# Kernel tuning notes

Hardware: AMD Instinct MI355X
Metric: run time of the kernel (lower is better)

Reference implementation:

```python
import jax, jax.numpy as jnp
import numpy as np

N_NODES = 50000
N_EDGES = 800000
IN_CH = 128
HID = 128
N_GRAPHS = 512


def setup_inputs() -> dict:
    key = jax.random.key(0)
    ks = jax.random.split(key, 12)
    x = jax.random.normal(ks[0], (N_NODES, IN_CH), dtype=jnp.float32)
    edge_index = jax.random.randint(ks[1], (2, N_EDGES), 0, N_NODES, dtype=jnp.int64)
    batch = jnp.sort(jax.random.randint(ks[2], (N_NODES,), 0, N_GRAPHS, dtype=jnp.int64))
    s = 0.05
    params = {
        'W1l': jax.random.normal(ks[3], (HID, IN_CH), dtype=jnp.float32) * s,
        'W1r': jax.random.normal(ks[4], (HID, IN_CH), dtype=jnp.float32) * s,
        'b1': jax.random.normal(ks[5], (HID,), dtype=jnp.float32) * s,
        'W2l': jax.random.normal(ks[6], (HID, HID), dtype=jnp.float32) * s,
        'W2r': jax.random.normal(ks[7], (HID, HID), dtype=jnp.float32) * s,
        'b2': jax.random.normal(ks[8], (HID,), dtype=jnp.float32) * s,
        'W3l': jax.random.normal(ks[9], (HID, HID), dtype=jnp.float32) * s,
        'W3r': jax.random.normal(ks[10], (HID, HID), dtype=jnp.float32) * s,
        'b3': jax.random.normal(ks[11], (HID,), dtype=jnp.float32) * s,
    }
    return {'x': x, 'edge_index': edge_index, 'batch': batch, **params}


def reference(x, edge_index, batch, W1l, W1r, b1, W2l, W2r, b2, W3l, W3r, b3):
    src = edge_index[0]
    dst = edge_index[1]
    n = x.shape[0]
    # in-degree for mean aggregation (nodes with no in-edges get 0 aggregate)
    deg = jax.ops.segment_sum(jnp.ones((src.shape[0],), x.dtype), dst, num_segments=n)
    inv_deg = (1.0 / jnp.maximum(deg, 1.0))[:, None]  # [N,1]

    def sage(h, Wl, Wr, b):
        # gather neighbor feats, scatter-mean to targets, then linear + root term
        agg = jax.ops.segment_sum(h[src], dst, num_segments=n) * inv_deg  # [N,d]
        return agg @ Wl.T + h @ Wr.T + b

    h = jax.nn.relu(sage(x, W1l, W1r, b1))
    h = jax.nn.relu(sage(h, W2l, W2r, b2))
    h = jax.nn.relu(sage(h, W3l, W3r, b3))

    # global mean pool over graph ids
    counts = jax.ops.segment_sum(jnp.ones((n,), h.dtype), batch, num_segments=N_GRAPHS)
    pooled = jax.ops.segment_sum(h, batch, num_segments=N_GRAPHS)
    return pooled / jnp.maximum(counts, 1.0)[:, None]
```

## Files before the change

kernel.cpp:

```cpp
#include <hip/hip_runtime.h>

#define N_NODES 50000
#define NP 50048
#define N_EDGES 800000
#define N_GRAPHS 512
#define F 128
#define SCAN_BLOCKS 196

typedef __bf16 bf16x8 __attribute__((ext_vector_type(8)));
typedef float f32x4 __attribute__((ext_vector_type(4)));
typedef unsigned short ushort_t;
typedef unsigned int uint_t;

__device__ inline ushort_t f2bf(float f) {
    uint_t u = __float_as_uint(f);
    u += 0x7FFFu + ((u >> 16) & 1u);
    return (ushort_t)(u >> 16);
}
__device__ inline float bf2f(ushort_t u) {
    return __uint_as_float(((uint_t)u) << 16);
}

__global__ __launch_bounds__(256) void k_castx(const float* __restrict__ x,
                                               ushort_t* __restrict__ X) {
    int i = (blockIdx.x * 256 + threadIdx.x) * 4;
    if (i >= NP * F) return;
    uint_t lo = 0, hi = 0;
    if (i < N_NODES * F) {
        float4 v = *(const float4*)&x[i];
        lo = (uint_t)f2bf(v.x) | ((uint_t)f2bf(v.y) << 16);
        hi = (uint_t)f2bf(v.z) | ((uint_t)f2bf(v.w) << 16);
    }
    *(uint2*)&X[i] = make_uint2(lo, hi);
}

__global__ __launch_bounds__(256) void k_castw(const float* __restrict__ w0,
                                               const float* __restrict__ w1,
                                               const float* __restrict__ w2,
                                               const float* __restrict__ w3,
                                               const float* __restrict__ w4,
                                               const float* __restrict__ w5,
                                               ushort_t* __restrict__ W) {
    int idx = blockIdx.x * 256 + threadIdx.x;
    if (idx >= 6 * 4096) return;
    int m = idx >> 12;
    int o = (idx & 4095) * 4;
    const float* src = w0;
    if (m == 1) src = w1; else if (m == 2) src = w2; else if (m == 3) src = w3;
    else if (m == 4) src = w4; else if (m == 5) src = w5;
    float4 v = *(const float4*)&src[o];
    uint_t lo = (uint_t)f2bf(v.x) | ((uint_t)f2bf(v.y) << 16);
    uint_t hi = (uint_t)f2bf(v.z) | ((uint_t)f2bf(v.w) << 16);
    *(uint2*)&W[m * 16384 + o] = make_uint2(lo, hi);
}

__global__ __launch_bounds__(256) void k_deg(const int* __restrict__ dst,
                                             int* __restrict__ deg) {
    int e = blockIdx.x * 256 + threadIdx.x;
    if (e < N_EDGES) atomicAdd(&deg[dst[e]], 1);
}

__global__ __launch_bounds__(256) void k_scan1(const int* __restrict__ deg,
                                               int* __restrict__ part) {
    __shared__ int s[256];
    int i = blockIdx.x * 256 + threadIdx.x;
    s[threadIdx.x] = (i < N_NODES) ? deg[i] : 0;
    __syncthreads();
#pragma unroll
    for (int st = 128; st > 0; st >>= 1) {
        if (threadIdx.x < st) s[threadIdx.x] += s[threadIdx.x + st];
        __syncthreads();
    }
    if (threadIdx.x == 0) part[blockIdx.x] = s[0];
}

__global__ void k_scan2(int* __restrict__ part, int* __restrict__ offs) {
    if (threadIdx.x == 0) {
        int acc = 0;
        for (int i = 0; i < SCAN_BLOCKS; i++) {
            int v = part[i];
            part[i] = acc;
            acc += v;
        }
        offs[N_NODES] = N_EDGES;
    }
}

__global__ __launch_bounds__(256) void k_scan3(const int* __restrict__ deg,
                                               const int* __restrict__ part,
                                               int* __restrict__ offs,
                                               int* __restrict__ cursor) {
    __shared__ int s[256];
    int tid = threadIdx.x;
    int i = blockIdx.x * 256 + tid;
    int v = (i < N_NODES) ? deg[i] : 0;
    s[tid] = v;
    __syncthreads();
#pragma unroll
    for (int st = 1; st < 256; st <<= 1) {
        int add = (tid >= st) ? s[tid - st] : 0;
        __syncthreads();
        s[tid] += add;
        __syncthreads();
    }
    if (i < N_NODES) {
        int off = s[tid] - v + part[blockIdx.x];
        offs[i] = off;
        cursor[i] = off;
    }
}

__global__ __launch_bounds__(256) void k_fill(const int* __restrict__ src,
                                              const int* __restrict__ dst,
                                              int* __restrict__ cursor,
                                              int* __restrict__ csr) {
    int e = blockIdx.x * 256 + threadIdx.x;
    if (e < N_EDGES) {
        int pos = atomicAdd(&cursor[dst[e]], 1);
        csr[pos] = src[e];
    }
}

__global__ __launch_bounds__(256) void k_gather(const ushort_t* __restrict__ h,
                                                const int* __restrict__ csr,
                                                const int* __restrict__ offs,
                                                ushort_t* __restrict__ agg) {
    int t = blockIdx.x * 256 + threadIdx.x;
    int n = t >> 4;
    int lane = t & 15;
    if (n >= N_NODES) return;
    int lo = offs[n], hi = offs[n + 1];
    const uint4* h4 = (const uint4*)h;
    float ax[8], ay[8];
#pragma unroll
    for (int j = 0; j < 8; j++) { ax[j] = 0.f; ay[j] = 0.f; }
    int i = lo;
    for (; i + 2 <= hi; i += 2) {
        int s0 = csr[i], s1 = csr[i + 1];
        uint4 v0 = h4[(size_t)s0 * 16 + lane];
        uint4 v1 = h4[(size_t)s1 * 16 + lane];
        ax[0] += __uint_as_float(v0.x << 16); ax[1] += __uint_as_float(v0.x & 0xFFFF0000u);
        ax[2] += __uint_as_float(v0.y << 16); ax[3] += __uint_as_float(v0.y & 0xFFFF0000u);
        ax[4] += __uint_as_float(v0.z << 16); ax[5] += __uint_as_float(v0.z & 0xFFFF0000u);
        ax[6] += __uint_as_float(v0.w << 16); ax[7] += __uint_as_float(v0.w & 0xFFFF0000u);
        ay[0] += __uint_as_float(v1.x << 16); ay[1] += __uint_as_float(v1.x & 0xFFFF0000u);
        ay[2] += __uint_as_float(v1.y << 16); ay[3] += __uint_as_float(v1.y & 0xFFFF0000u);
        ay[4] += __uint_as_float(v1.z << 16); ay[5] += __uint_as_float(v1.z & 0xFFFF0000u);
        ay[6] += __uint_as_float(v1.w << 16); ay[7] += __uint_as_float(v1.w & 0xFFFF0000u);
    }
    if (i < hi) {
        int s0 = csr[i];
        uint4 v0 = h4[(size_t)s0 * 16 + lane];
        ax[0] += __uint_as_float(v0.x << 16); ax[1] += __uint_as_float(v0.x & 0xFFFF0000u);
        ax[2] += __uint_as_float(v0.y << 16); ax[3] += __uint_as_float(v0.y & 0xFFFF0000u);
        ax[4] += __uint_as_float(v0.z << 16); ax[5] += __uint_as_float(v0.z & 0xFFFF0000u);
        ax[6] += __uint_as_float(v0.w << 16); ax[7] += __uint_as_float(v0.w & 0xFFFF0000u);
    }
    float sc = 1.0f / fmaxf((float)(hi - lo), 1.0f);
    uint_t r[4];
#pragma unroll
    for (int j = 0; j < 4; j++) {
        ushort_t e0 = f2bf((ax[2 * j] + ay[2 * j]) * sc);
        ushort_t e1 = f2bf((ax[2 * j + 1] + ay[2 * j + 1]) * sc);
        r[j] = (uint_t)e0 | ((uint_t)e1 << 16);
    }
    ((uint4*)agg)[(size_t)n * 16 + lane] = make_uint4(r[0], r[1], r[2], r[3]);
}

__global__ __launch_bounds__(256) void k_linear(const ushort_t* __restrict__ agg,
                                                const ushort_t* h,
                                                const ushort_t* __restrict__ Wl,
                                                const ushort_t* __restrict__ Wr,
                                                const float* __restrict__ bias,
                                                ushort_t* out) {
    __shared__ uint4 Alds4[512];
    __shared__ uint4 Blds4[512];
    ushort_t* Alds = (ushort_t*)Alds4;
    ushort_t* Blds = (ushort_t*)Blds4;

    int t = threadIdx.x;
    int w = t >> 6;
    int lane = t & 63;
    int bm = blockIdx.x * 128;
    int wm = (w & 1) * 64;
    int wn = (w >> 1) * 64;
    int lrow = lane & 15;
    int kg = lane >> 4;

    f32x4 acc[4][4];
#pragma unroll
    for (int i = 0; i < 4; i++)
#pragma unroll
        for (int j = 0; j < 4; j++) acc[i][j] = (f32x4){0.f, 0.f, 0.f, 0.f};

    for (int kk = 0; kk < 256; kk += 32) {
        const ushort_t* A = (kk < 128) ? agg : h;
        const ushort_t* W = (kk < 128) ? Wl : Wr;
        int k0 = kk & 127;

        __syncthreads();
#pragma unroll
        for (int p = 0; p < 2; p++) {
            int s = p * 256 + t;
            int chunk = s >> 7;
            int row = s & 127;
            const ushort_t* gA = A + (size_t)(bm + row) * F + k0 + chunk * 8;
            const ushort_t* gB = W + (size_t)row * F + k0 + chunk * 8;
            ushort_t* lA = Alds + (size_t)((p * 4 + w) * 64) * 8;
            ushort_t* lB = Blds + (size_t)((p * 4 + w) * 64) * 8;
            __builtin_amdgcn_global_load_lds(
                (const __attribute__((address_space(1))) void*)gA,
                (__attribute__((address_space(3))) void*)lA, 16, 0, 0);
            __builtin_amdgcn_global_load_lds(
                (const __attribute__((address_space(1))) void*)gB,
                (__attribute__((address_space(3))) void*)lB, 16, 0, 0);
        }
        __syncthreads();

        bf16x8 af[4], bfr[4];
#pragma unroll
        for (int i = 0; i < 4; i++)
            af[i] = *(const bf16x8*)(Alds + (size_t)(kg * 128 + wm + i * 16 + lrow) * 8);
#pragma unroll
        for (int j = 0; j < 4; j++)
            bfr[j] = *(const bf16x8*)(Blds + (size_t)(kg * 128 + wn + j * 16 + lrow) * 8);
#pragma unroll
        for (int i = 0; i < 4; i++)
#pragma unroll
            for (int j = 0; j < 4; j++)
                acc[i][j] = __builtin_amdgcn_mfma_f32_16x16x32_bf16(
                    af[i], bfr[j], acc[i][j], 0, 0, 0);
    }

    int quad = lane >> 4;
#pragma unroll
    for (int j = 0; j < 4; j++) {
        int c = wn + j * 16 + lrow;
        float bj = bias[c];
#pragma unroll
        for (int i = 0; i < 4; i++) {
#pragma unroll
            for (int r = 0; r < 4; r++) {
                int row = bm + wm + i * 16 + quad * 4 + r;
                if (row < N_NODES) {
                    float v = fmaxf(acc[i][j][r] + bj, 0.0f);
                    out[(size_t)row * F + c] = f2bf(v);
                }
            }
        }
    }
}

__global__ __launch_bounds__(128) void k_pool(const ushort_t* __restrict__ h,
                                              const int* __restrict__ batch,
                                              float* __restrict__ out) {
    int g = blockIdx.x;
    int j = threadIdx.x;
    int lo = 0, hi = N_NODES;
    while (lo < hi) {
        int m = (lo + hi) >> 1;
        if (batch[m] < g) lo = m + 1; else hi = m;
    }
    int start = lo;
    lo = start; hi = N_NODES;
    while (lo < hi) {
        int m = (lo + hi) >> 1;
        if (batch[m] < g + 1) lo = m + 1; else hi = m;
    }
    int end = lo;
    float s = 0.0f;
    for (int n = start; n < end; n++) s += bf2f(h[(size_t)n * F + j]);
    out[g * F + j] = s / fmaxf((float)(end - start), 1.0f);
}

extern "C" void kernel_launch(void* const* d_in, const int* in_sizes, int n_in,
                              void* d_out, int out_size, void* d_ws, size_t ws_size,
                              hipStream_t stream) {
    const float* x   = (const float*)d_in[0];
    const int*   ei  = (const int*)d_in[1];
    const int* batch = (const int*)d_in[2];
    const float* W1l = (const float*)d_in[3];
    const float* W1r = (const float*)d_in[4];
    const float* b1  = (const float*)d_in[5];
    const float* W2l = (const float*)d_in[6];
    const float* W2r = (const float*)d_in[7];
    const float* b2  = (const float*)d_in[8];
    const float* W3l = (const float*)d_in[9];
    const float* W3r = (const float*)d_in[10];
    const float* b3  = (const float*)d_in[11];
    float* out = (float*)d_out;

    const int* src = ei;
    const int* dst = ei + N_EDGES;

    ushort_t* X   = (ushort_t*)d_ws;
    ushort_t* H   = X + (size_t)NP * F;
    ushort_t* AGG = H + (size_t)NP * F;
    ushort_t* WB  = AGG + (size_t)NP * F;
    int* iw = (int*)(WB + 6 * 16384);
    int* ideg   = iw;
    int* offs   = ideg + N_NODES;
    int* cursor = offs + N_NODES + 1;
    int* part   = cursor + N_NODES;
    int* csr    = part + 256;

    const ushort_t* Wb1l = WB;
    const ushort_t* Wb1r = WB + 16384;
    const ushort_t* Wb2l = WB + 2 * 16384;
    const ushort_t* Wb2r = WB + 3 * 16384;
    const ushort_t* Wb3l = WB + 4 * 16384;
    const ushort_t* Wb3r = WB + 5 * 16384;

    k_castx<<<(NP * F / 4 + 255) / 256, 256, 0, stream>>>(x, X);
    k_castw<<<(6 * 4096 + 255) / 256, 256, 0, stream>>>(W1l, W1r, W2l, W2r, W3l, W3r, WB);

    hipMemsetAsync(ideg, 0, N_NODES * sizeof(int), stream);
    k_deg<<<(N_EDGES + 255) / 256, 256, 0, stream>>>(dst, ideg);
    k_scan1<<<SCAN_BLOCKS, 256, 0, stream>>>(ideg, part);
    k_scan2<<<1, 64, 0, stream>>>(part, offs);
    k_scan3<<<SCAN_BLOCKS, 256, 0, stream>>>(ideg, part, offs, cursor);
    k_fill<<<(N_EDGES + 255) / 256, 256, 0, stream>>>(src, dst, cursor, csr);

    const int gatherBlocks = (N_NODES * 16 + 255) / 256;
    const int linearBlocks = NP / 128;

    k_gather<<<gatherBlocks, 256, 0, stream>>>(X, csr, offs, AGG);
    k_linear<<<linearBlocks, 256, 0, stream>>>(AGG, X, Wb1l, Wb1r, b1, H);
    k_gather<<<gatherBlocks, 256, 0, stream>>>(H, csr, offs, AGG);
    k_linear<<<linearBlocks, 256, 0, stream>>>(AGG, H, Wb2l, Wb2r, b2, H);
    k_gather<<<gatherBlocks, 256, 0, stream>>>(H, csr, offs, AGG);
    k_linear<<<linearBlocks, 256, 0, stream>>>(AGG, H, Wb3l, Wb3r, b3, H);

    k_pool<<<N_GRAPHS, 128, 0, stream>>>(H, batch, out);
}
```

Before: 378.4 us.

## Fuse prep kernels, unroll gather by four, retile linear to 64-row blocks

Merges the x cast, weight cast and degree-count kernels into one launch to cut launch overhead. The gather loop now issues four neighbour row loads per iteration instead of two, giving more memory-level parallelism. The linear kernel moves to 64-row tiles with a K-step of 64, doubling the block count and halving the per-wave accumulator count. The cost is a larger B tile in LDS and more B-tile reloads per output row.

```diff
diff --git a/kernel.cpp b/kernel.cpp
--- a/kernel.cpp
+++ b/kernel.cpp
@@ -6,6 +6,9 @@
 #define N_GRAPHS 512
 #define F 128
 #define SCAN_BLOCKS 196
+#define CASTX_BLOCKS 6256
+#define CASTW_BLOCKS 96
+#define DEG_BLOCKS 3125
 
 typedef __bf16 bf16x8 __attribute__((ext_vector_type(8)));
 typedef float f32x4 __attribute__((ext_vector_type(4)));
@@ -21,43 +24,40 @@
     return __uint_as_float(((uint_t)u) << 16);
 }
 
-__global__ __launch_bounds__(256) void k_castx(const float* __restrict__ x,
-                                               ushort_t* __restrict__ X) {
-    int i = (blockIdx.x * 256 + threadIdx.x) * 4;
-    if (i >= NP * F) return;
-    uint_t lo = 0, hi = 0;
-    if (i < N_NODES * F) {
-        float4 v = *(const float4*)&x[i];
-        lo = (uint_t)f2bf(v.x) | ((uint_t)f2bf(v.y) << 16);
-        hi = (uint_t)f2bf(v.z) | ((uint_t)f2bf(v.w) << 16);
-    }
-    *(uint2*)&X[i] = make_uint2(lo, hi);
-}
-
-__global__ __launch_bounds__(256) void k_castw(const float* __restrict__ w0,
-                                               const float* __restrict__ w1,
-                                               const float* __restrict__ w2,
-                                               const float* __restrict__ w3,
-                                               const float* __restrict__ w4,
-                                               const float* __restrict__ w5,
-                                               ushort_t* __restrict__ W) {
-    int idx = blockIdx.x * 256 + threadIdx.x;
-    if (idx >= 6 * 4096) return;
-    int m = idx >> 12;
-    int o = (idx & 4095) * 4;
-    const float* src = w0;
-    if (m == 1) src = w1; else if (m == 2) src = w2; else if (m == 3) src = w3;
-    else if (m == 4) src = w4; else if (m == 5) src = w5;
-    float4 v = *(const float4*)&src[o];
-    uint_t lo = (uint_t)f2bf(v.x) | ((uint_t)f2bf(v.y) << 16);
-    uint_t hi = (uint_t)f2bf(v.z) | ((uint_t)f2bf(v.w) << 16);
-    *(uint2*)&W[m * 16384 + o] = make_uint2(lo, hi);
-}
-
-__global__ __launch_bounds__(256) void k_deg(const int* __restrict__ dst,
-                                             int* __restrict__ deg) {
-    int e = blockIdx.x * 256 + threadIdx.x;
-    if (e < N_EDGES) atomicAdd(&deg[dst[e]], 1);
+__global__ __launch_bounds__(256) void k_prep(
+    const float* __restrict__ x,
+    const float* __restrict__ w0, const float* __restrict__ w1,
+    const float* __restrict__ w2, const float* __restrict__ w3,
+    const float* __restrict__ w4, const float* __restrict__ w5,
+    const int* __restrict__ dst,
+    ushort_t* __restrict__ X, ushort_t* __restrict__ WB,
+    int* __restrict__ ideg) {
+    int b = blockIdx.x;
+    int t = threadIdx.x;
+    if (b < CASTX_BLOCKS) {
+        int i = (b * 256 + t) * 4;
+        uint_t lo = 0, hi = 0;
+        if (i < N_NODES * F) {
+            float4 v = *(const float4*)&x[i];
+            lo = (uint_t)f2bf(v.x) | ((uint_t)f2bf(v.y) << 16);
+            hi = (uint_t)f2bf(v.z) | ((uint_t)f2bf(v.w) << 16);
+        }
+        *(uint2*)&X[i] = make_uint2(lo, hi);
+    } else if (b < CASTX_BLOCKS + CASTW_BLOCKS) {
+        int idx = (b - CASTX_BLOCKS) * 256 + t;
+        int m = idx >> 12;
+        int o = (idx & 4095) * 4;
+        const float* src = w0;
+        if (m == 1) src = w1; else if (m == 2) src = w2; else if (m == 3) src = w3;
+        else if (m == 4) src = w4; else if (m == 5) src = w5;
+        float4 v = *(const float4*)&src[o];
+        uint_t lo = (uint_t)f2bf(v.x) | ((uint_t)f2bf(v.y) << 16);
+        uint_t hi = (uint_t)f2bf(v.z) | ((uint_t)f2bf(v.w) << 16);
+        *(uint2*)&WB[m * 16384 + o] = make_uint2(lo, hi);
+    } else {
+        int e = (b - CASTX_BLOCKS - CASTW_BLOCKS) * 256 + t;
+        atomicAdd(&ideg[dst[e]], 1);
+    }
 }
 
 __global__ __launch_bounds__(256) void k_scan1(const int* __restrict__ deg,
@@ -119,6 +119,13 @@
         int pos = atomicAdd(&cursor[dst[e]], 1);
         csr[pos] = src[e];
     }
+}
+
+__device__ inline void addrow(float* a, uint4 v) {
+    a[0] += __uint_as_float(v.x << 16); a[1] += __uint_as_float(v.x & 0xFFFF0000u);
+    a[2] += __uint_as_float(v.y << 16); a[3] += __uint_as_float(v.y & 0xFFFF0000u);
+    a[4] += __uint_as_float(v.z << 16); a[5] += __uint_as_float(v.z & 0xFFFF0000u);
+    a[6] += __uint_as_float(v.w << 16); a[7] += __uint_as_float(v.w & 0xFFFF0000u);
 }
 
 __global__ __launch_bounds__(256) void k_gather(const ushort_t* __restrict__ h,
@@ -135,26 +142,18 @@
 #pragma unroll
     for (int j = 0; j < 8; j++) { ax[j] = 0.f; ay[j] = 0.f; }
     int i = lo;
-    for (; i + 2 <= hi; i += 2) {
-        int s0 = csr[i], s1 = csr[i + 1];
+    for (; i + 4 <= hi; i += 4) {
+        int s0 = csr[i], s1 = csr[i + 1], s2 = csr[i + 2], s3 = csr[i + 3];
         uint4 v0 = h4[(size_t)s0 * 16 + lane];
         uint4 v1 = h4[(size_t)s1 * 16 + lane];
-        ax[0] += __uint_as_float(v0.x << 16); ax[1] += __uint_as_float(v0.x & 0xFFFF0000u);
-        ax[2] += __uint_as_float(v0.y << 16); ax[3] += __uint_as_float(v0.y & 0xFFFF0000u);
-        ax[4] += __uint_as_float(v0.z << 16); ax[5] += __uint_as_float(v0.z & 0xFFFF0000u);
-        ax[6] += __uint_as_float(v0.w << 16); ax[7] += __uint_as_float(v0.w & 0xFFFF0000u);
-        ay[0] += __uint_as_float(v1.x << 16); ay[1] += __uint_as_float(v1.x & 0xFFFF0000u);
-        ay[2] += __uint_as_float(v1.y << 16); ay[3] += __uint_as_float(v1.y & 0xFFFF0000u);
-        ay[4] += __uint_as_float(v1.z << 16); ay[5] += __uint_as_float(v1.z & 0xFFFF0000u);
-        ay[6] += __uint_as_float(v1.w << 16); ay[7] += __uint_as_float(v1.w & 0xFFFF0000u);
-    }
-    if (i < hi) {
+        uint4 v2 = h4[(size_t)s2 * 16 + lane];
+        uint4 v3 = h4[(size_t)s3 * 16 + lane];
+        addrow(ax, v0); addrow(ay, v1); addrow(ax, v2); addrow(ay, v3);
+    }
+    for (; i < hi; i++) {
         int s0 = csr[i];
         uint4 v0 = h4[(size_t)s0 * 16 + lane];
-        ax[0] += __uint_as_float(v0.x << 16); ax[1] += __uint_as_float(v0.x & 0xFFFF0000u);
-        ax[2] += __uint_as_float(v0.y << 16); ax[3] += __uint_as_float(v0.y & 0xFFFF0000u);
-        ax[4] += __uint_as_float(v0.z << 16); ax[5] += __uint_as_float(v0.z & 0xFFFF0000u);
-        ax[6] += __uint_as_float(v0.w << 16); ax[7] += __uint_as_float(v0.w & 0xFFFF0000u);
+        addrow(ax, v0);
     }
     float sc = 1.0f / fmaxf((float)(hi - lo), 1.0f);
     uint_t r[4];
@@ -174,26 +173,27 @@
                                                 const float* __restrict__ bias,
                                                 ushort_t* out) {
     __shared__ uint4 Alds4[512];
-    __shared__ uint4 Blds4[512];
+    __shared__ uint4 Blds4[1024];
     ushort_t* Alds = (ushort_t*)Alds4;
     ushort_t* Blds = (ushort_t*)Blds4;
 
     int t = threadIdx.x;
     int w = t >> 6;
     int lane = t & 63;
-    int bm = blockIdx.x * 128;
-    int wm = (w & 1) * 64;
+    int bm = blockIdx.x * 64;
+    int wm = (w & 1) * 32;
     int wn = (w >> 1) * 64;
     int lrow = lane & 15;
     int kg = lane >> 4;
 
-    f32x4 acc[4][4];
-#pragma unroll
-    for (int i = 0; i < 4; i++)
+    f32x4 acc[2][4];
+#pragma unroll
+    for (int i = 0; i < 2; i++)
 #pragma unroll
         for (int j = 0; j < 4; j++) acc[i][j] = (f32x4){0.f, 0.f, 0.f, 0.f};
 
-    for (int kk = 0; kk < 256; kk += 32) {
+    for (int iter = 0; iter < 4; iter++) {
+        int kk = iter * 64;
         const ushort_t* A = (kk < 128) ? agg : h;
         const ushort_t* W = (kk < 128) ? Wl : Wr;
         int k0 = kk & 127;
@@ -201,35 +201,43 @@
         __syncthreads();
 #pragma unroll
         for (int p = 0; p < 2; p++) {
-            int s = p * 256 + t;
-            int chunk = s >> 7;
-            int row = s & 127;
-            const ushort_t* gA = A + (size_t)(bm + row) * F + k0 + chunk * 8;
-            const ushort_t* gB = W + (size_t)row * F + k0 + chunk * 8;
-            ushort_t* lA = Alds + (size_t)((p * 4 + w) * 64) * 8;
-            ushort_t* lB = Blds + (size_t)((p * 4 + w) * 64) * 8;
+            int chunkA = p * 4 + w;
+            const ushort_t* gA = A + (size_t)(bm + lane) * F + k0 + chunkA * 8;
+            ushort_t* lA = Alds + (size_t)(chunkA * 64) * 8;
             __builtin_amdgcn_global_load_lds(
                 (const __attribute__((address_space(1))) void*)gA,
                 (__attribute__((address_space(3))) void*)lA, 16, 0, 0);
+        }
+#pragma unroll
+        for (int p = 0; p < 4; p++) {
+            int chunkB = p * 2 + (w >> 1);
+            int rbase = (w & 1) * 64;
+            const ushort_t* gB = W + (size_t)(rbase + lane) * F + k0 + chunkB * 8;
+            ushort_t* lB = Blds + (size_t)(chunkB * 128 + rbase) * 8;
             __builtin_amdgcn_global_load_lds(
                 (const __attribute__((address_space(1))) void*)gB,
                 (__attribute__((address_space(3))) void*)lB, 16, 0, 0);
         }
         __syncthreads();
 
-        bf16x8 af[4], bfr[4];
-#pragma unroll
-        for (int i = 0; i < 4; i++)
-            af[i] = *(const bf16x8*)(Alds + (size_t)(kg * 128 + wm + i * 16 + lrow) * 8);
-#pragma unroll
-        for (int j = 0; j < 4; j++)
-            bfr[j] = *(const bf16x8*)(Blds + (size_t)(kg * 128 + wn + j * 16 + lrow) * 8);
-#pragma unroll
-        for (int i = 0; i < 4; i++)
+#pragma unroll
+        for (int ks = 0; ks < 2; ks++) {
+            bf16x8 af[2], bfr[4];
+#pragma unroll
+            for (int i = 0; i < 2; i++)
+                af[i] = *(const bf16x8*)(Alds +
+                    (size_t)((ks * 4 + kg) * 64 + wm + i * 16 + lrow) * 8);
 #pragma unroll
             for (int j = 0; j < 4; j++)
-                acc[i][j] = __builtin_amdgcn_mfma_f32_16x16x32_bf16(
-                    af[i], bfr[j], acc[i][j], 0, 0, 0);
+                bfr[j] = *(const bf16x8*)(Blds +
+                    (size_t)((ks * 4 + kg) * 128 + wn + j * 16 + lrow) * 8);
+#pragma unroll
+            for (int i = 0; i < 2; i++)
+#pragma unroll
+                for (int j = 0; j < 4; j++)
+                    acc[i][j] = __builtin_amdgcn_mfma_f32_16x16x32_bf16(
+                        af[i], bfr[j], acc[i][j], 0, 0, 0);
+        }
     }
 
     int quad = lane >> 4;
@@ -238,7 +246,7 @@
         int c = wn + j * 16 + lrow;
         float bj = bias[c];
 #pragma unroll
-        for (int i = 0; i < 4; i++) {
+        for (int i = 0; i < 2; i++) {
 #pragma unroll
             for (int r = 0; r < 4; r++) {
                 int row = bm + wm + i * 16 + quad * 4 + r;
@@ -311,18 +319,16 @@
     const ushort_t* Wb3l = WB + 4 * 16384;
     const ushort_t* Wb3r = WB + 5 * 16384;
 
-    k_castx<<<(NP * F / 4 + 255) / 256, 256, 0, stream>>>(x, X);
-    k_castw<<<(6 * 4096 + 255) / 256, 256, 0, stream>>>(W1l, W1r, W2l, W2r, W3l, W3r, WB);
-
     hipMemsetAsync(ideg, 0, N_NODES * sizeof(int), stream);
-    k_deg<<<(N_EDGES + 255) / 256, 256, 0, stream>>>(dst, ideg);
+    k_prep<<<CASTX_BLOCKS + CASTW_BLOCKS + DEG_BLOCKS, 256, 0, stream>>>(
+        x, W1l, W1r, W2l, W2r, W3l, W3r, dst, X, WB, ideg);
     k_scan1<<<SCAN_BLOCKS, 256, 0, stream>>>(ideg, part);
     k_scan2<<<1, 64, 0, stream>>>(part, offs);
     k_scan3<<<SCAN_BLOCKS, 256, 0, stream>>>(ideg, part, offs, cursor);
     k_fill<<<(N_EDGES + 255) / 256, 256, 0, stream>>>(src, dst, cursor, csr);
 
     const int gatherBlocks = (N_NODES * 16 + 255) / 256;
-    const int linearBlocks = NP / 128;
+    const int linearBlocks = NP / 64;
 
     k_gather<<<gatherBlocks, 256, 0, stream>>>(X, csr, offs, AGG);
     k_linear<<<linearBlocks, 256, 0, stream>>>(AGG, X, Wb1l, Wb1r, b1, H);
```

Result: faster. 361.8 us (-4.4%).
